# Kernel optimization log

Hardware: AMD Instinct MI355X
Metric: run time of the kernel (lower is better)

The kernel has to match this reference:

```python
import jax, jax.numpy as jnp
import numpy as np
from functools import partial
from jax import lax

B, K, CLIP_DIM, SBERT_DIM, D_MODEL, R_RANK, ATTN_DIM, PMAX = 128, 1024, 768, 384, 256, 64, 256, 8
RHO = 0.35

def _normalize(x, axis=-1, eps=1e-12):
    return x / jnp.maximum(jnp.linalg.norm(x, axis=axis, keepdims=True), eps)

def _build_graph():
    rng = np.random.default_rng(0)
    pid = np.zeros((K, PMAX), np.int32)
    pm = np.zeros((K, PMAX), bool)
    for i in range(K - 1):  # node i's parents are in (i, K); root = K-1 has none
        n = int(rng.integers(1, PMAX + 1))
        n = min(n, K - 1 - i)
        cands = rng.choice(np.arange(i + 1, K), size=n, replace=False)
        pid[i, :n] = cands
        pm[i, :n] = True
    order = np.arange(K - 1, -1, -1, dtype=np.int32)  # parents before children
    return jnp.asarray(pid), jnp.asarray(pm), jnp.asarray(order)

def setup_inputs() -> dict:
    key = jax.random.key(0)
    ks = iter(jax.random.split(key, 32))
    r = lambda shape, s=0.02: jax.random.normal(next(ks), shape, jnp.float32) * s
    pid, pm, order = _build_graph()
    return {
        "t_clip": jax.random.normal(next(ks), (B, CLIP_DIM), jnp.float32),
        "v_clip": jax.random.normal(next(ks), (B, CLIP_DIM), jnp.float32),
        "concept_sbert": jax.random.normal(next(ks), (K, SBERT_DIM), jnp.float32),
        "Wt": r((CLIP_DIM, D_MODEL)), "bt": jnp.zeros((D_MODEL,)),
        "Wv": r((CLIP_DIM, D_MODEL)), "bv": jnp.zeros((D_MODEL,)),
        "Wc": r((SBERT_DIM, D_MODEL)), "bc": jnp.zeros((D_MODEL,)),
        "Wp1": r((3 * D_MODEL, 2 * D_MODEL)), "bp1": jnp.zeros((2 * D_MODEL,)),
        "Wp2": r((2 * D_MODEL, D_MODEL)), "bp2": jnp.zeros((D_MODEL,)),
        "Wm1": r((3 * D_MODEL, 2 * D_MODEL)), "bm1": jnp.zeros((2 * D_MODEL,)),
        "Wm2": r((2 * D_MODEL, D_MODEL)), "bm2": jnp.zeros((D_MODEL,)),
        "tau_logits": jnp.zeros((K,)),
        "U": r((D_MODEL, R_RANK)), "V": r((D_MODEL, R_RANK)),
        "Wg1": r((SBERT_DIM, R_RANK)), "bg1": jnp.zeros((R_RANK,)),
        "Wg2": r((R_RANK, R_RANK)), "bg2": jnp.zeros((R_RANK,)),
        "w_out": r((K, R_RANK)), "b_out": jnp.zeros((K,)),
        "concept_q": r((K, ATTN_DIM)),
        "parents_idx": pid, "parents_mask": pm, "order": order,
    }

def _forward(t_clip, v_clip, concept_sbert, Wt, bt, Wv, bv, Wc, bc,
             Wp1, bp1, Wp2, bp2, Wm1, bm1, Wm2, bm2, tau_logits,
             U, V, Wg1, bg1, Wg2, bg2, w_out, b_out, concept_q,
             parents_idx, parents_mask, order):
    gelu = partial(jax.nn.gelu, approximate=False)  # torch nn.GELU default = exact erf
    t = _normalize(t_clip) @ Wt + bt                 # [B, D]
    v = _normalize(v_clip) @ Wv + bv                 # [B, D]
    d = concept_sbert @ Wc + bc                      # [K, D]
    # x = [v, t, d] broadcast to [B, K, 3D]
    x = jnp.concatenate([
        jnp.broadcast_to(v[:, None, :], (t.shape[0], K, D_MODEL)),
        jnp.broadcast_to(t[:, None, :], (t.shape[0], K, D_MODEL)),
        jnp.broadcast_to(d[None, :, :], (t.shape[0], K, D_MODEL)),
    ], axis=-1)
    h_plus = gelu(x @ Wp1 + bp1) @ Wp2 + bp2
    h_minus = gelu(x @ Wm1 + bm1) @ Wm2 + bm2
    tau = jax.nn.sigmoid(tau_logits)[None, :, None]
    h = tau * h_plus + (1.0 - tau) * h_minus         # [B, K, D]
    u = jnp.einsum('bkd,dr->bkr', h, U)
    vv = jnp.einsum('bkd,dr->bkr', h, V)
    g = gelu(concept_sbert @ Wg1 + bg1) @ Wg2 + bg2  # [K, R]
    inter = u * vv * g[None, :, :]
    logits = jnp.einsum('bkr,kr->bk', inter, w_out) + b_out[None, :]
    p = jax.nn.sigmoid(logits)                        # [B, K]
    # --- top-down hierarchical attention + multiplicative aggregation ---
    q = _normalize(concept_q)                         # [K, A]
    def step(p_hat, node):
        par = parents_idx[node]                       # [P] int
        m = parents_mask[node]                        # [P] bool
        scores = jnp.where(m, q[par] @ q[node], -1e9)
        alpha = jax.nn.softmax(scores)                # [P]
        vals = p_hat[:, par]                          # [B, P] gather of parent probs
        prod = jnp.prod(jnp.where(m[None, :], alpha[None, :] * vals, 1.0), axis=-1)
        new = jnp.where(m.any(), RHO * p[:, node] + (1.0 - RHO) * prod, p_hat[:, node])
        return p_hat.at[:, node].set(new), None       # scatter write
    p_hat, _ = lax.scan(step, p, order)
    return p_hat

def reference(t_clip, v_clip, concept_sbert, Wt, bt, Wv, bv, Wc, bc,
              Wp1, bp1, Wp2, bp2, Wm1, bm1, Wm2, bm2, tau_logits,
              U, V, Wg1, bg1, Wg2, bg2, w_out, b_out, concept_q,
              parents_idx, parents_mask, order):
    return _forward(t_clip, v_clip, concept_sbert, Wt, bt, Wv, bv, Wc, bc,
                    Wp1, bp1, Wp2, bp2, Wm1, bm1, Wm2, bm2, tau_logits,
                    U, V, Wg1, bg1, Wg2, bg2, w_out, b_out, concept_q,
                    parents_idx, parents_mask, order)
```

## Files before the change

### kernel.cpp

```cpp
#include <hip/hip_runtime.h>
#include <math.h>

typedef __attribute__((ext_vector_type(8))) short short8;
typedef __attribute__((ext_vector_type(4))) float float4v;
typedef __attribute__((ext_vector_type(2))) float float2v;

struct P {
  const float *t_clip, *v_clip, *sbert;
  const float *Wt, *bt, *Wv, *bv, *Wc, *bc;
  const float *Wp1, *bp1, *Wp2, *bp2, *Wm1, *bm1, *Wm2, *bm2;
  const float *tau_logits, *U, *V, *Wg1, *bg1, *Wg2, *bg2, *w_out, *b_out, *concept_q;
  const int *pid;
  float *vt32;
  unsigned short *vtbf;
  unsigned short *dbf;
  unsigned short *w1upP, *w1upM;
  unsigned short *w1lowP, *w1lowM;
  unsigned short *Ctp, *Ctm;
  unsigned short *Wpk, *Wmk;
  float *Ap, *Am;
  float *biasPM, *tau, *gw, *aprod;
  unsigned short *parS;
  int *sorted, *lvlStart, *nlev;
  float *pOut;
};

__device__ __forceinline__ unsigned short bf16ru(float f) {
    unsigned u = __float_as_uint(f);
    u += 0x7fffu + ((u >> 16) & 1u);
    return (unsigned short)(u >> 16);
}

__device__ __forceinline__ void glds16(const void* g, void* l) {
    __builtin_amdgcn_global_load_lds((const __attribute__((address_space(1))) unsigned int*)g,
                                     (__attribute__((address_space(3))) unsigned int*)l, 16, 0, 0);
}

__device__ __forceinline__ unsigned packpair(float2v a, unsigned c) {
    float2v cb;
    cb.x = __uint_as_float(c << 16);
    cb.y = __uint_as_float(c & 0xffff0000u);
    float2v x = a + cb;
    float2v t = x * x;
    float2v i = t * (-0.06649038f) + 0.39894228f;
    float2v p = x * i + 0.5f;
    float2v g = x * p;
    union { float2v f; unsigned u[2]; } gu; gu.f = g;
    return __builtin_amdgcn_perm(gu.u[1], gu.u[0], 0x07060302u);
}


__device__ void tv_f(const P& a, int rel, float* sm) {
    int sel = rel & 1, bt8 = rel >> 1;
    float* xrow = sm;
    float* scale = sm + 6144;
    int tid = threadIdx.x;
    const float* X = sel ? a.t_clip : a.v_clip;
    int b0 = bt8 * 8;
    for (int r = 0; r < 8; ++r)
        for (int i = tid; i < 768; i += 256)
            xrow[r * 768 + i] = X[(size_t)(b0 + r) * 768 + i];
    __syncthreads();
    {
        int r = tid >> 5, l = tid & 31;
        float ss = 0.f;
        for (int i = l; i < 768; i += 32) { float v = xrow[r * 768 + i]; ss = fmaf(v, v, ss); }
        for (int mk = 16; mk; mk >>= 1) ss += __shfl_xor(ss, mk);
        if (l == 0) scale[r] = 1.0f / fmaxf(sqrtf(ss), 1e-12f);
    }
    __syncthreads();
    int col4 = (tid & 63) * 4, rg = tid >> 6;
    const float* W = sel ? a.Wt : a.Wv;
    const float* bias = sel ? a.bt : a.bv;
    float acc[2][4] = {};
    const float* xr0 = xrow + (rg * 2) * 768;
    const float* xr1 = xr0 + 768;
    for (int d = 0; d < 768; ++d) {
        float4 w = *(const float4*)&W[(size_t)d * 256 + col4];
        float x0 = xr0[d], x1 = xr1[d];
        acc[0][0] = fmaf(x0, w.x, acc[0][0]); acc[0][1] = fmaf(x0, w.y, acc[0][1]);
        acc[0][2] = fmaf(x0, w.z, acc[0][2]); acc[0][3] = fmaf(x0, w.w, acc[0][3]);
        acc[1][0] = fmaf(x1, w.x, acc[1][0]); acc[1][1] = fmaf(x1, w.y, acc[1][1]);
        acc[1][2] = fmaf(x1, w.z, acc[1][2]); acc[1][3] = fmaf(x1, w.w, acc[1][3]);
    }
    float4 bb = *(const float4*)&bias[col4];
    int vtcol = sel * 256 + col4;
#pragma unroll
    for (int rr = 0; rr < 2; ++rr) {
        int b = b0 + rg * 2 + rr;
        float sc = scale[rg * 2 + rr];
        float4 o;
        o.x = acc[rr][0] * sc + bb.x; o.y = acc[rr][1] * sc + bb.y;
        o.z = acc[rr][2] * sc + bb.z; o.w = acc[rr][3] * sc + bb.w;
        *(float4*)&a.vt32[(size_t)b * 512 + vtcol] = o;
        ushort4 ob;
        ob.x = bf16ru(o.x); ob.y = bf16ru(o.y); ob.z = bf16ru(o.z); ob.w = bf16ru(o.w);
        size_t idx = (size_t)(b >> 4) * 8192 + (vtcol >> 5) * 512 + ((vtcol >> 3) & 3) * 128
                   + (b & 15) * 8 + (vtcol & 7);
        *(ushort4*)&a.vtbf[idx] = ob;
    }
}

__device__ void d_f(const P& a, int rel, float* sm) {
    int r0 = rel * 8;
    int tid = threadIdx.x;
    for (int i = tid; i < 3072; i += 256) sm[i] = a.sbert[(size_t)r0 * 384 + i];
    __syncthreads();
    int col4 = (tid & 63) * 4, rg = tid >> 6;
    float acc[2][4] = {};
    const float* x0p = sm + (rg * 2) * 384;
    const float* x1p = x0p + 384;
    for (int d = 0; d < 384; ++d) {
        float4 w = *(const float4*)&a.Wc[(size_t)d * 256 + col4];
        float x0 = x0p[d], x1 = x1p[d];
        acc[0][0] = fmaf(x0, w.x, acc[0][0]); acc[0][1] = fmaf(x0, w.y, acc[0][1]);
        acc[0][2] = fmaf(x0, w.z, acc[0][2]); acc[0][3] = fmaf(x0, w.w, acc[0][3]);
        acc[1][0] = fmaf(x1, w.x, acc[1][0]); acc[1][1] = fmaf(x1, w.y, acc[1][1]);
        acc[1][2] = fmaf(x1, w.z, acc[1][2]); acc[1][3] = fmaf(x1, w.w, acc[1][3]);
    }
    float4 bb = *(const float4*)&a.bc[col4];
#pragma unroll
    for (int rr = 0; rr < 2; ++rr) {
        int row = r0 + rg * 2 + rr;
        ushort4 ob;
        ob.x = bf16ru(acc[rr][0] + bb.x); ob.y = bf16ru(acc[rr][1] + bb.y);
        ob.z = bf16ru(acc[rr][2] + bb.z); ob.w = bf16ru(acc[rr][3] + bb.w);
        size_t idx = (size_t)(row >> 4) * 4096 + (col4 >> 5) * 512 + ((col4 >> 3) & 3) * 128
                   + (row & 15) * 8 + (col4 & 7);
        *(ushort4*)&a.dbf[idx] = ob;
    }
}

__device__ void wcv_f(const P& a, int rel, float* smf) {
    unsigned short* wl = (unsigned short*)smf;
    int mat = rel & 1, rb = rel >> 1;
    int r0 = rb * 16;
    const float* W1 = mat ? a.Wm1 : a.Wp1;
    int tid = threadIdx.x;
    for (int it = 0; it < 8; ++it) {
        int i4 = (it * 256 + tid) * 4;
        float4 w = *(const float4*)&W1[(size_t)r0 * 512 + i4];
        ushort4 o;
        o.x = bf16ru(w.x); o.y = bf16ru(w.y); o.z = bf16ru(w.z); o.w = bf16ru(w.w);
        *(ushort4*)&wl[i4] = o;
    }
    __syncthreads();
    unsigned short* dst; int K16, kbase;
    if (r0 < 512) { dst = mat ? a.w1upM : a.w1upP;  K16 = 8192; kbase = r0; }
    else          { dst = mat ? a.w1lowM : a.w1lowP; K16 = 4096; kbase = r0 - 512; }
    for (int i = tid; i < 1024; i += 256) {
        int kg = i >> 9, n = i & 511;
        int k0 = kbase + kg * 8;
        ushort4 o0, o1;
        o0.x = wl[(kg * 8 + 0) * 512 + n]; o0.y = wl[(kg * 8 + 1) * 512 + n];
        o0.z = wl[(kg * 8 + 2) * 512 + n]; o0.w = wl[(kg * 8 + 3) * 512 + n];
        o1.x = wl[(kg * 8 + 4) * 512 + n]; o1.y = wl[(kg * 8 + 5) * 512 + n];
        o1.z = wl[(kg * 8 + 6) * 512 + n]; o1.w = wl[(kg * 8 + 7) * 512 + n];
        size_t off = (size_t)(n >> 4) * K16 + (k0 >> 5) * 512 + ((k0 >> 3) & 3) * 128 + (n & 15) * 8;
        *(ushort4*)&dst[off]     = o0;
        *(ushort4*)&dst[off + 4] = o1;
    }
}

__device__ void packW_f(const P& a, int rel, float* smf) {
    float* w2l = smf;
    int mat = rel >> 6, jb = rel & 63;
    int j0 = jb * 8;
    const float* W2 = mat ? a.Wm2 : a.Wp2;
    unsigned short* outP = mat ? a.Wmk : a.Wpk;
    int tid = threadIdx.x;
    for (int i = tid; i < 2048; i += 256) w2l[i] = W2[(size_t)j0 * 256 + i];
    __syncthreads();
    int c = tid & 127, jg = tid >> 7;
    float acc[4] = {};
    const float* uv = (c < 64) ? (a.U + c) : (a.V + (c - 64));
    for (int d = 0; d < 256; ++d) {
        float u = uv[(size_t)d * 64];
        const float* wr = w2l + (jg * 4) * 256 + d;
        acc[0] = fmaf(wr[0],   u, acc[0]);
        acc[1] = fmaf(wr[256], u, acc[1]);
        acc[2] = fmaf(wr[512], u, acc[2]);
        acc[3] = fmaf(wr[768], u, acc[3]);
    }
#pragma unroll
    for (int r = 0; r < 4; ++r) {
        int j = j0 + jg * 4 + r;
        size_t o = (size_t)(j >> 5) * 4096 + (c >> 4) * 512 + ((j >> 3) & 3) * 128 + (c & 15) * 8 + (j & 7);
        outP[o] = bf16ru(acc[r]);
    }
}

__device__ void gw_f(const P& a, int rel, float* sm) {
    float* sb = sm;
    float* hid = sm + 6144;
    int k0 = rel * 16;
    int tid = threadIdx.x;
    for (int i = tid; i < 6144; i += 256) sb[i] = a.sbert[(size_t)k0 * 384 + i];
    __syncthreads();
    int col = tid & 63, rg = tid >> 6;
    float bg = a.bg1[col];
    float acc[4] = {bg, bg, bg, bg};
    for (int d = 0; d < 384; ++d) {
        float w = a.Wg1[(size_t)d * 64 + col];
        const float* xr = sb + (rg * 4) * 384 + d;
        acc[0] = fmaf(xr[0],    w, acc[0]);
        acc[1] = fmaf(xr[384],  w, acc[1]);
        acc[2] = fmaf(xr[768],  w, acc[2]);
        acc[3] = fmaf(xr[1152], w, acc[3]);
    }
#pragma unroll
    for (int r = 0; r < 4; ++r)
        hid[(rg * 4 + r) * 64 + col] = 0.5f * acc[r] * (1.0f + erff(acc[r] * 0.7071067811865475f));
    __syncthreads();
    float bg2v = a.bg2[col];
    float a2[4] = {bg2v, bg2v, bg2v, bg2v};
    for (int d = 0; d < 64; ++d) {
        float w = a.Wg2[(size_t)d * 64 + col];
        const float* hr = hid + (rg * 4) * 64 + d;
        a2[0] = fmaf(hr[0],   w, a2[0]);
        a2[1] = fmaf(hr[64],  w, a2[1]);
        a2[2] = fmaf(hr[128], w, a2[2]);
        a2[3] = fmaf(hr[192], w, a2[3]);
    }
#pragma unroll
    for (int r = 0; r < 4; ++r) {
        int k = k0 + rg * 4 + r;
        a.gw[(size_t)k * 64 + col] = a2[r] * a.w_out[(size_t)k * 64 + col];
    }
}

__device__ void alpha_f(const P& a, int blk) {
    int t = threadIdx.x, wv = t >> 6, lane = t & 63;
    int node = blk * 4 + wv;
    int slot = lane >> 3, e = lane & 7;
    int par = a.pid[node * 8 + slot];
    const float4* qk = (const float4*)(a.concept_q + (size_t)node * 256);
    const float4* qp = (const float4*)(a.concept_q + (size_t)par * 256);
    float dq = 0, np = 0, ns = 0;
#pragma unroll
    for (int i = 0; i < 8; ++i) {
        float4 x = qp[e * 8 + i], y = qk[e * 8 + i];
        dq += x.x * y.x + x.y * y.y + x.z * y.z + x.w * y.w;
        np += x.x * x.x + x.y * x.y + x.z * x.z + x.w * x.w;
        ns += y.x * y.x + y.y * y.y + y.z * y.z + y.w * y.w;
    }
#pragma unroll
    for (int mk = 1; mk <= 4; mk <<= 1) {
        dq += __shfl_xor(dq, mk); np += __shfl_xor(np, mk); ns += __shfl_xor(ns, mk);
    }
    float score = dq / fmaxf(sqrtf(np) * sqrtf(ns), 1e-24f);
    float sc[8]; int pv[8];
#pragma unroll
    for (int s = 0; s < 8; ++s) { sc[s] = __shfl(score, s * 8); pv[s] = __shfl(par, s * 8); }
    float mx = -1e30f;
#pragma unroll
    for (int s = 0; s < 8; ++s) if (pv[s] != 0) mx = fmaxf(mx, sc[s]);
    float sum = 0.f;
#pragma unroll
    for (int s = 0; s < 8; ++s) sum += (pv[s] != 0) ? expf(sc[s] - mx) : 0.0f;
    float ap = 1.0f;
#pragma unroll
    for (int s = 0; s < 8; ++s) if (pv[s] != 0) ap *= expf(sc[s] - mx) / sum;
    if (lane == 0) a.aprod[node] = ap;
    if (e == 0) a.parS[node * 8 + slot] = (par != 0) ? (unsigned short)par : (unsigned short)1024;
}

__device__ void misc_f(const P& a, int g) {
    int t = threadIdx.x;
    if (g == 0) {
        int c = t & 127;
        const float* bb = (t < 128) ? a.bp2 : a.bm2;
        const float* uv = (c < 64) ? (a.U + c) : (a.V + (c - 64));
        float acc = 0.f;
        for (int d = 0; d < 256; ++d) acc = fmaf(bb[d], uv[(size_t)d * 64], acc);
        a.biasPM[t] = acc;
    } else {
        int k = (g - 1) * 256 + t;
        a.tau[k] = 1.0f / (1.0f + expf(-a.tau_logits[k]));
    }
}

__device__ void levels_f(const P& a, int* smemI) {
    volatile int* lvl = smemI;
    int* cnt  = smemI + 1024;
    int* ofs  = smemI + 2048;
    int* ping = smemI + 3072;
    int* pong = smemI + 3328;
    int* mflag = smemI + 3584;
    int t = threadIdx.x;
    int par[4][8]; int hasm[4];
#pragma unroll
    for (int r = 0; r < 4; ++r) {
        int n = t * 4 + r, h = 0;
#pragma unroll
        for (int s = 0; s < 8; ++s) { int p = a.pid[n * 8 + s]; par[r][s] = p; h |= (p != 0); }
        hasm[r] = h; lvl[n] = 0;
    }
    if (t == 0) mflag[1] = 0;
    __syncthreads();
    for (int round = 0; round < 200; ++round) {
        if (t == 0) mflag[0] = 0;
        __syncthreads();
        int ch = 0;
        for (int sub = 0; sub < 8; ++sub) {
#pragma unroll
            for (int r = 0; r < 4; ++r) {
                if (!hasm[r]) continue;
                int mx = 0;
#pragma unroll
                for (int s = 0; s < 8; ++s) { int p = par[r][s]; if (p) mx = max(mx, lvl[p]); }
                int nl = mx + 1;
                if (nl > lvl[t * 4 + r]) { lvl[t * 4 + r] = nl; ch = 1; }
            }
        }
        if (ch) mflag[0] = 1;
        __syncthreads();
        if (mflag[0] == 0) break;
    }
    int lm = 0;
    for (int r = 0; r < 4; ++r) lm = max(lm, lvl[t * 4 + r]);
    atomicMax(&mflag[1], lm);
    for (int r = 0; r < 4; ++r) cnt[t * 4 + r] = 0;
    __syncthreads();
    for (int r = 0; r < 4; ++r) atomicAdd(&cnt[lvl[t * 4 + r]], 1);
    __syncthreads();
    int c0 = cnt[t * 4], c1 = cnt[t * 4 + 1], c2 = cnt[t * 4 + 2], c3 = cnt[t * 4 + 3];
    ping[t] = c0 + c1 + c2 + c3;
    __syncthreads();
    int* src = ping; int* dst = pong;
    for (int off = 1; off < 256; off <<= 1) {
        int v = src[t];
        if (t >= off) v += src[t - off];
        dst[t] = v;
        __syncthreads();
        int* tmp = src; src = dst; dst = tmp;
    }
    int excl = (t == 0) ? 0 : src[t - 1];
    ofs[t * 4] = excl; ofs[t * 4 + 1] = excl + c0;
    ofs[t * 4 + 2] = excl + c0 + c1; ofs[t * 4 + 3] = excl + c0 + c1 + c2;
#pragma unroll
    for (int r = 0; r < 4; ++r) a.lvlStart[t * 4 + r] = ofs[t * 4 + r];
    if (t == 0) { a.lvlStart[1024] = 1024; a.nlev[0] = mflag[1] + 1; }
    __syncthreads();
    for (int r = 0; r < 4; ++r) {
        int n = t * 4 + r;
        int pos = atomicAdd(&ofs[lvl[n]], 1);
        a.sorted[pos] = n;
    }
}

__global__ void __launch_bounds__(256) prep1_kernel(P a) {
    __shared__ float smem[7200];
    int bid = blockIdx.x;
    if (bid == 0) { levels_f(a, (int*)smem); return; }
    bid -= 1;
    if (bid < 32) { tv_f(a, bid, smem); return; }
    bid -= 32;
    if (bid < 128) { d_f(a, bid, smem); return; }
    bid -= 128;
    if (bid < 96) { wcv_f(a, bid, smem); return; }
    bid -= 96;
    if (bid < 128) { packW_f(a, bid, smem); return; }
    bid -= 128;
    if (bid < 64) { gw_f(a, bid, smem); return; }
    bid -= 64;
    if (bid < 256) { alpha_f(a, bid); return; }
    bid -= 256;
    misc_f(a, bid);
}

__global__ void __launch_bounds__(256) prep2_kernel(P a) {
    int bid = blockIdx.x;
    int tid = threadIdx.x;
    int wv = tid >> 6, lane = tid & 63;
    int m = lane & 15, quad = lane >> 4;
    if (bid < 256) {
        int mat = bid & 1, mt = (bid >> 1) & 15, ntile = bid >> 5;
        const unsigned short* A = a.dbf + (size_t)(mt * 4 + wv) * 4096 + quad * 128 + m * 8;
        const unsigned short* B = (mat ? a.w1lowM : a.w1lowP) + (size_t)quad * 128 + m * 8;
        unsigned short* Ct = mat ? a.Ctm : a.Ctp;
        float4v acc[4];
#pragma unroll
        for (int i = 0; i < 4; ++i) acc[i] = (float4v)0.0f;
        for (int s = 0; s < 8; ++s) {
            short8 af = *(const short8*)(A + s * 512);
#pragma unroll
            for (int nt = 0; nt < 4; ++nt) {
                short8 bf = *(const short8*)(B + (size_t)(ntile * 4 + nt) * 4096 + s * 512);
                acc[nt] = __builtin_amdgcn_mfma_f32_16x16x32_bf16(af, bf, acc[nt], 0, 0, 0);
            }
        }
        int rowg = mt * 4 + wv;
        int rl = quad * 4;
#pragma unroll
        for (int nt = 0; nt < 4; ++nt) {
            int j = ntile * 64 + nt * 16 + m;
            size_t base = (size_t)rowg * 8192 + (j >> 5) * 512 + ((j >> 3) & 3) * 128 + (j & 7);
#pragma unroll
            for (int rr = 0; rr < 4; ++rr)
                Ct[base + (rl + rr) * 8] = bf16ru(acc[nt][rr]);
        }
    } else {
        int rel = bid - 256;
        int mat = rel & 1, mt = (rel >> 1) & 1, ntile = rel >> 2;
        const unsigned short* A = a.vtbf + (size_t)(mt * 4 + wv) * 8192 + quad * 128 + m * 8;
        const unsigned short* B = (mat ? a.w1upM : a.w1upP) + (size_t)quad * 128 + m * 8;
        const float* bias = mat ? a.bm1 : a.bp1;
        float* out = mat ? a.Am : a.Ap;
        float4v acc[4];
#pragma unroll
        for (int i = 0; i < 4; ++i) acc[i] = (float4v)0.0f;
        for (int s = 0; s < 16; ++s) {
            short8 af = *(const short8*)(A + s * 512);
#pragma unroll
            for (int nt = 0; nt < 4; ++nt) {
                short8 bf = *(const short8*)(B + (size_t)(ntile * 4 + nt) * 8192 + s * 512);
                acc[nt] = __builtin_amdgcn_mfma_f32_16x16x32_bf16(af, bf, acc[nt], 0, 0, 0);
            }
        }
        int b0r = mt * 64 + wv * 16 + quad * 4;
#pragma unroll
        for (int nt = 0; nt < 4; ++nt) {
            int j = ntile * 64 + nt * 16 + m;
            float bb = bias[j];
#pragma unroll
            for (int rr = 0; rr < 4; ++rr)
                out[(size_t)(b0r + rr) * 512 + j] = acc[nt][rr] + bb;
        }
    }
}

__global__ void __launch_bounds__(512, 2) main_kernel(P a) {
    __shared__ float apL[4096];
    __shared__ char wbuf[2][16384];
    int tid = threadIdx.x;
    int wv2 = tid >> 6, lane = tid & 63;
    int mat = wv2 >> 2, sub = wv2 & 3;
    int m = lane & 15, quad = lane >> 4;
    int b0 = (blockIdx.x >> 4) * 4;
    int k0 = (blockIdx.x & 15) << 6;

    for (int i = tid; i < 1024; i += 512) {
        int arr = i >> 7, off = i & 127;
        const float* src = ((arr >> 2) ? a.Am : a.Ap) + (size_t)(b0 + (arr & 3)) * 512;
        ((float4*)apL)[i] = ((const float4*)src)[off];
    }

    const char* wg = ((wv2 < 4) ? (const char*)a.Wpk : (const char*)a.Wmk)
                   + (wv2 & 3) * 2048 + lane * 16;
    char* wl0 = &wbuf[0][wv2 * 2048];
    char* wl1 = &wbuf[1][wv2 * 2048];

    const unsigned short* Ct = mat ? a.Ctm : a.Ctp;
    const float* aL = apL + mat * 2048;
    int kt = (k0 >> 4) + sub;
    const char* ctB = (const char*)Ct + (size_t)kt * 16384 + quad * 256 + m * 16;

    float4v acc[4][8];
#pragma unroll
    for (int b = 0; b < 4; ++b)
#pragma unroll
        for (int i = 0; i < 8; ++i) acc[b][i] = (float4v)0.0f;

    glds16(wg, wl0);
    glds16(wg + 1024, wl0 + 1024);
    uint4 crN = *(const uint4*)(ctB);
    __syncthreads();

    for (int n = 0; n < 16; ++n) {
        if (n < 15) {
            char* dst = ((n + 1) & 1) ? wl1 : wl0;
            glds16(wg + (n + 1) * 8192, dst);
            glds16(wg + (n + 1) * 8192 + 1024, dst + 1024);
        }
        uint4 cr = crN;
        if (n < 15) crN = *(const uint4*)(ctB + (n + 1) * 1024);
        union { uint4 u; short8 s; } fa[4];
        const float* aj = aL + n * 32 + quad * 8;
#pragma unroll
        for (int b = 0; b < 4; ++b) {
            float4v x0 = *(const float4v*)(aj + b * 512);
            float4v x1 = *(const float4v*)(aj + b * 512 + 4);
            float2v v;
            v.x = x0[0]; v.y = x0[1]; fa[b].u.x = packpair(v, cr.x);
            v.x = x0[2]; v.y = x0[3]; fa[b].u.y = packpair(v, cr.y);
            v.x = x1[0]; v.y = x1[1]; fa[b].u.z = packpair(v, cr.z);
            v.x = x1[2]; v.y = x1[3]; fa[b].u.w = packpair(v, cr.w);
        }
        const char* wB = &wbuf[n & 1][0] + mat * 8192 + quad * 256 + m * 16;
#pragma unroll
        for (int nt = 0; nt < 8; ++nt) {
            short8 wf = *(const short8*)(wB + nt * 1024);
            acc[0][nt] = __builtin_amdgcn_mfma_f32_16x16x32_bf16(fa[0].s, wf, acc[0][nt], 0, 0, 0);
            acc[1][nt] = __builtin_amdgcn_mfma_f32_16x16x32_bf16(fa[1].s, wf, acc[1][nt], 0, 0, 0);
            acc[2][nt] = __builtin_amdgcn_mfma_f32_16x16x32_bf16(fa[2].s, wf, acc[2][nt], 0, 0, 0);
            acc[3][nt] = __builtin_amdgcn_mfma_f32_16x16x32_bf16(fa[3].s, wf, acc[3][nt], 0, 0, 0);
        }
        __syncthreads();
    }

    float* xbuf = (float*)wbuf;
    int kk[4]; float tv[4];
#pragma unroll
    for (int r = 0; r < 4; ++r) { kk[r] = k0 + sub * 16 + quad * 4 + r; tv[r] = a.tau[kk[r]]; }
    float lsum[4][4] = {};
#pragma unroll
    for (int t4 = 0; t4 < 4; ++t4) {
        __syncthreads();
        if (mat == 1) {
#pragma unroll
            for (int b = 0; b < 4; ++b) {
                int slot = (sub * 4 + b) * 64 + lane;
#pragma unroll
                for (int r = 0; r < 4; ++r) {
                    xbuf[r * 1024 + slot]       = acc[b][t4][r];
                    xbuf[(r + 4) * 1024 + slot] = acc[b][t4 + 4][r];
                }
            }
        }
        __syncthreads();
        if (mat == 0) {
            int cU = t4 * 16 + m, cV = cU + 64;
            float bPu = a.biasPM[cU], bMu = a.biasPM[128 + cU];
            float bPv = a.biasPM[cV], bMv = a.biasPM[128 + cV];
#pragma unroll
            for (int b = 0; b < 4; ++b) {
                int slot = (sub * 4 + b) * 64 + lane;
#pragma unroll
                for (int r = 0; r < 4; ++r) {
                    float g = a.gw[(size_t)kk[r] * 64 + cU];
                    float u  = tv[r] * (acc[b][t4][r] + bPu)
                             + (1.0f - tv[r]) * (xbuf[r * 1024 + slot] + bMu);
                    float vx = tv[r] * (acc[b][t4 + 4][r] + bPv)
                             + (1.0f - tv[r]) * (xbuf[(r + 4) * 1024 + slot] + bMv);
                    lsum[b][r] = fmaf(u * vx, g, lsum[b][r]);
                }
            }
        }
    }
    if (mat == 0) {
#pragma unroll
        for (int r = 0; r < 4; ++r) {
            float bo = a.b_out[kk[r]];
#pragma unroll
            for (int b = 0; b < 4; ++b) {
                float s = lsum[b][r];
                s += __shfl_xor(s, 1); s += __shfl_xor(s, 2); s += __shfl_xor(s, 4); s += __shfl_xor(s, 8);
                if (m == 0)
                    a.pOut[(size_t)(b0 + b) * 1024 + kk[r]] = 1.0f / (1.0f + expf(-(s + bo)));
            }
        }
    }
}

#define PH_STRIDE 1056
__global__ void __launch_bounds__(256) scan_kernel(P a) {
    __shared__ float ph[4 * PH_STRIDE];
    __shared__ float aprodL[1024];
    __shared__ unsigned short parL[8192];
    __shared__ short sortedL[1024];
    __shared__ int lvlStartL[1025];
    int t = threadIdx.x;
    int b0 = blockIdx.x * 4;
    for (int i = t; i < 1024; i += 256) ((uint4*)parL)[i] = ((const uint4*)a.parS)[i];
    for (int i = t; i < 1024; i += 256) {
        aprodL[i] = a.aprod[i];
        sortedL[i] = (short)a.sorted[i];
        lvlStartL[i] = a.lvlStart[i];
    }
    if (t == 0) lvlStartL[1024] = 1024;
    for (int i = t; i < 4096; i += 256) {
        int bb = i >> 10, k = i & 1023;
        ph[bb * PH_STRIDE + k] = a.pOut[(size_t)(b0 + bb) * 1024 + k];
    }
    if (t < 4) ph[t * PH_STRIDE + 1024] = 1.0f;
    __syncthreads();
    int nlev = a.nlev[0];
    int w = t >> 6, lane = t & 63;
    float* myph = ph + w * PH_STRIDE;
    for (int L = 1; L < nlev; ++L) {
        int s0 = lvlStartL[L], s1 = lvlStartL[L + 1];
        for (int i = s0 + lane; i < s1; i += 64) {
            int node = sortedL[i];
            ushort4 pA = *(const ushort4*)&parL[node * 8];
            ushort4 pB = *(const ushort4*)&parL[node * 8 + 4];
            float prod = aprodL[node];
            prod *= myph[pA.x] * myph[pA.y];
            prod *= myph[pA.z] * myph[pA.w];
            prod *= myph[pB.x] * myph[pB.y];
            prod *= myph[pB.z] * myph[pB.w];
            myph[node] = fmaf(0.35f, myph[node], 0.65f * prod);
        }
    }
    __syncthreads();
    for (int i = t; i < 4096; i += 256) {
        int bb = i >> 10, k = i & 1023;
        a.pOut[(size_t)(b0 + bb) * 1024 + k] = ph[bb * PH_STRIDE + k];
    }
}

extern "C" void kernel_launch(void* const* d_in, const int* in_sizes, int n_in,
                              void* d_out, int out_size, void* d_ws, size_t ws_size,
                              hipStream_t stream) {
    P a;
    a.t_clip = (const float*)d_in[0];
    a.v_clip = (const float*)d_in[1];
    a.sbert  = (const float*)d_in[2];
    a.Wt  = (const float*)d_in[3];  a.bt  = (const float*)d_in[4];
    a.Wv  = (const float*)d_in[5];  a.bv  = (const float*)d_in[6];
    a.Wc  = (const float*)d_in[7];  a.bc  = (const float*)d_in[8];
    a.Wp1 = (const float*)d_in[9];  a.bp1 = (const float*)d_in[10];
    a.Wp2 = (const float*)d_in[11]; a.bp2 = (const float*)d_in[12];
    a.Wm1 = (const float*)d_in[13]; a.bm1 = (const float*)d_in[14];
    a.Wm2 = (const float*)d_in[15]; a.bm2 = (const float*)d_in[16];
    a.tau_logits = (const float*)d_in[17];
    a.U   = (const float*)d_in[18]; a.V   = (const float*)d_in[19];
    a.Wg1 = (const float*)d_in[20]; a.bg1 = (const float*)d_in[21];
    a.Wg2 = (const float*)d_in[22]; a.bg2 = (const float*)d_in[23];
    a.w_out = (const float*)d_in[24]; a.b_out = (const float*)d_in[25];
    a.concept_q = (const float*)d_in[26];
    a.pid = (const int*)d_in[27];

    char* w = (char*)d_ws;
    a.vt32   = (float*)(w + 0);
    a.vtbf   = (unsigned short*)(w + 262144);
    a.dbf    = (unsigned short*)(w + 393216);
    a.w1upP  = (unsigned short*)(w + 917504);
    a.w1upM  = (unsigned short*)(w + 1441792);
    a.w1lowP = (unsigned short*)(w + 1966080);
    a.w1lowM = (unsigned short*)(w + 2228224);
    a.Ctp    = (unsigned short*)(w + 2490368);
    a.Ctm    = (unsigned short*)(w + 3538944);
    a.Wpk    = (unsigned short*)(w + 4587520);
    a.Wmk    = (unsigned short*)(w + 4718592);
    a.Ap     = (float*)(w + 4849664);
    a.Am     = (float*)(w + 5111808);
    a.biasPM = (float*)(w + 5373952);
    a.tau    = (float*)(w + 5374976);
    a.gw     = (float*)(w + 5379072);
    a.parS   = (unsigned short*)(w + 5641216);
    a.aprod  = (float*)(w + 5657600);
    a.sorted = (int*)(w + 5661696);
    a.lvlStart = (int*)(w + 5665792);
    a.nlev     = (int*)(w + 5670144);
    a.pOut = (float*)d_out;

    prep1_kernel<<<710, 256, 0, stream>>>(a);
    prep2_kernel<<<288, 256, 0, stream>>>(a);
    main_kernel<<<512, 512, 0, stream>>>(a);
    scan_kernel<<<32, 256, 0, stream>>>(a);
}
```

Baseline: 261.8 us.

## Move prep projections from scalar FP32 loops to bf16 MFMA GEMMs

```diff
diff --git a/kernel.cpp b/kernel.cpp
--- a/kernel.cpp
+++ b/kernel.cpp
@@ -11,15 +11,23 @@
   const float *Wp1, *bp1, *Wp2, *bp2, *Wm1, *bm1, *Wm2, *bm2;
   const float *tau_logits, *U, *V, *Wg1, *bg1, *Wg2, *bg2, *w_out, *b_out, *concept_q;
   const int *pid;
-  float *vt32;
+  unsigned short *tvbf;
+  unsigned short *sbbf;
+  unsigned short *wtvB;
+  unsigned short *wcB;
+  unsigned short *wg1B;
+  unsigned short *wg2B;
+  unsigned short *w2bf;
+  unsigned short *uvB;
+  unsigned short *w1upP, *w1upM;
+  unsigned short *w1lowP, *w1lowM;
   unsigned short *vtbf;
   unsigned short *dbf;
-  unsigned short *w1upP, *w1upM;
-  unsigned short *w1lowP, *w1lowM;
+  unsigned short *ghbf;
   unsigned short *Ctp, *Ctm;
   unsigned short *Wpk, *Wmk;
   float *Ap, *Am;
-  float *biasPM, *tau, *gw, *aprod;
+  float *sBuf, *biasPM, *tau, *gw, *aprod;
   unsigned short *parS;
   int *sorted, *lvlStart, *nlev;
   float *pOut;
@@ -50,183 +58,116 @@
 }
 
 
-__device__ void tv_f(const P& a, int rel, float* sm) {
-    int sel = rel & 1, bt8 = rel >> 1;
-    float* xrow = sm;
-    float* scale = sm + 6144;
+__device__ void bconv_f(const float* __restrict__ srcRow0, unsigned short* __restrict__ dst,
+                        int N, int K16, int kbase, char* smc) {
+    unsigned short* wl = (unsigned short*)smc;
     int tid = threadIdx.x;
-    const float* X = sel ? a.t_clip : a.v_clip;
-    int b0 = bt8 * 8;
-    for (int r = 0; r < 8; ++r)
-        for (int i = tid; i < 768; i += 256)
-            xrow[r * 768 + i] = X[(size_t)(b0 + r) * 768 + i];
-    __syncthreads();
-    {
-        int r = tid >> 5, l = tid & 31;
-        float ss = 0.f;
-        for (int i = l; i < 768; i += 32) { float v = xrow[r * 768 + i]; ss = fmaf(v, v, ss); }
-        for (int mk = 16; mk; mk >>= 1) ss += __shfl_xor(ss, mk);
-        if (l == 0) scale[r] = 1.0f / fmaxf(sqrtf(ss), 1e-12f);
-    }
-    __syncthreads();
-    int col4 = (tid & 63) * 4, rg = tid >> 6;
-    const float* W = sel ? a.Wt : a.Wv;
-    const float* bias = sel ? a.bt : a.bv;
-    float acc[2][4] = {};
-    const float* xr0 = xrow + (rg * 2) * 768;
-    const float* xr1 = xr0 + 768;
-    for (int d = 0; d < 768; ++d) {
-        float4 w = *(const float4*)&W[(size_t)d * 256 + col4];
-        float x0 = xr0[d], x1 = xr1[d];
-        acc[0][0] = fmaf(x0, w.x, acc[0][0]); acc[0][1] = fmaf(x0, w.y, acc[0][1]);
-        acc[0][2] = fmaf(x0, w.z, acc[0][2]); acc[0][3] = fmaf(x0, w.w, acc[0][3]);
-        acc[1][0] = fmaf(x1, w.x, acc[1][0]); acc[1][1] = fmaf(x1, w.y, acc[1][1]);
-        acc[1][2] = fmaf(x1, w.z, acc[1][2]); acc[1][3] = fmaf(x1, w.w, acc[1][3]);
-    }
-    float4 bb = *(const float4*)&bias[col4];
-    int vtcol = sel * 256 + col4;
-#pragma unroll
-    for (int rr = 0; rr < 2; ++rr) {
-        int b = b0 + rg * 2 + rr;
-        float sc = scale[rg * 2 + rr];
-        float4 o;
-        o.x = acc[rr][0] * sc + bb.x; o.y = acc[rr][1] * sc + bb.y;
-        o.z = acc[rr][2] * sc + bb.z; o.w = acc[rr][3] * sc + bb.w;
-        *(float4*)&a.vt32[(size_t)b * 512 + vtcol] = o;
-        ushort4 ob;
-        ob.x = bf16ru(o.x); ob.y = bf16ru(o.y); ob.z = bf16ru(o.z); ob.w = bf16ru(o.w);
-        size_t idx = (size_t)(b >> 4) * 8192 + (vtcol >> 5) * 512 + ((vtcol >> 3) & 3) * 128
-                   + (b & 15) * 8 + (vtcol & 7);
-        *(ushort4*)&a.vtbf[idx] = ob;
-    }
-}
-
-__device__ void d_f(const P& a, int rel, float* sm) {
-    int r0 = rel * 8;
-    int tid = threadIdx.x;
-    for (int i = tid; i < 3072; i += 256) sm[i] = a.sbert[(size_t)r0 * 384 + i];
-    __syncthreads();
-    int col4 = (tid & 63) * 4, rg = tid >> 6;
-    float acc[2][4] = {};
-    const float* x0p = sm + (rg * 2) * 384;
-    const float* x1p = x0p + 384;
-    for (int d = 0; d < 384; ++d) {
-        float4 w = *(const float4*)&a.Wc[(size_t)d * 256 + col4];
-        float x0 = x0p[d], x1 = x1p[d];
-        acc[0][0] = fmaf(x0, w.x, acc[0][0]); acc[0][1] = fmaf(x0, w.y, acc[0][1]);
-        acc[0][2] = fmaf(x0, w.z, acc[0][2]); acc[0][3] = fmaf(x0, w.w, acc[0][3]);
-        acc[1][0] = fmaf(x1, w.x, acc[1][0]); acc[1][1] = fmaf(x1, w.y, acc[1][1]);
-        acc[1][2] = fmaf(x1, w.z, acc[1][2]); acc[1][3] = fmaf(x1, w.w, acc[1][3]);
-    }
-    float4 bb = *(const float4*)&a.bc[col4];
-#pragma unroll
-    for (int rr = 0; rr < 2; ++rr) {
-        int row = r0 + rg * 2 + rr;
-        ushort4 ob;
-        ob.x = bf16ru(acc[rr][0] + bb.x); ob.y = bf16ru(acc[rr][1] + bb.y);
-        ob.z = bf16ru(acc[rr][2] + bb.z); ob.w = bf16ru(acc[rr][3] + bb.w);
-        size_t idx = (size_t)(row >> 4) * 4096 + (col4 >> 5) * 512 + ((col4 >> 3) & 3) * 128
-                   + (row & 15) * 8 + (col4 & 7);
-        *(ushort4*)&a.dbf[idx] = ob;
-    }
-}
-
-__device__ void wcv_f(const P& a, int rel, float* smf) {
-    unsigned short* wl = (unsigned short*)smf;
-    int mat = rel & 1, rb = rel >> 1;
-    int r0 = rb * 16;
-    const float* W1 = mat ? a.Wm1 : a.Wp1;
-    int tid = threadIdx.x;
-    for (int it = 0; it < 8; ++it) {
-        int i4 = (it * 256 + tid) * 4;
-        float4 w = *(const float4*)&W1[(size_t)r0 * 512 + i4];
+    int tot4 = 4 * N;
+    for (int i4 = tid; i4 < tot4; i4 += 256) {
+        float4 w = ((const float4*)srcRow0)[i4];
         ushort4 o;
         o.x = bf16ru(w.x); o.y = bf16ru(w.y); o.z = bf16ru(w.z); o.w = bf16ru(w.w);
-        *(ushort4*)&wl[i4] = o;
-    }
-    __syncthreads();
-    unsigned short* dst; int K16, kbase;
-    if (r0 < 512) { dst = mat ? a.w1upM : a.w1upP;  K16 = 8192; kbase = r0; }
-    else          { dst = mat ? a.w1lowM : a.w1lowP; K16 = 4096; kbase = r0 - 512; }
-    for (int i = tid; i < 1024; i += 256) {
-        int kg = i >> 9, n = i & 511;
+        *(ushort4*)&wl[i4 * 4] = o;
+    }
+    __syncthreads();
+    for (int i = tid; i < 2 * N; i += 256) {
+        int kg = (i >= N) ? 1 : 0;
+        int n = i - kg * N;
         int k0 = kbase + kg * 8;
         ushort4 o0, o1;
-        o0.x = wl[(kg * 8 + 0) * 512 + n]; o0.y = wl[(kg * 8 + 1) * 512 + n];
-        o0.z = wl[(kg * 8 + 2) * 512 + n]; o0.w = wl[(kg * 8 + 3) * 512 + n];
-        o1.x = wl[(kg * 8 + 4) * 512 + n]; o1.y = wl[(kg * 8 + 5) * 512 + n];
-        o1.z = wl[(kg * 8 + 6) * 512 + n]; o1.w = wl[(kg * 8 + 7) * 512 + n];
+        o0.x = wl[(kg * 8 + 0) * N + n]; o0.y = wl[(kg * 8 + 1) * N + n];
+        o0.z = wl[(kg * 8 + 2) * N + n]; o0.w = wl[(kg * 8 + 3) * N + n];
+        o1.x = wl[(kg * 8 + 4) * N + n]; o1.y = wl[(kg * 8 + 5) * N + n];
+        o1.z = wl[(kg * 8 + 6) * N + n]; o1.w = wl[(kg * 8 + 7) * N + n];
         size_t off = (size_t)(n >> 4) * K16 + (k0 >> 5) * 512 + ((k0 >> 3) & 3) * 128 + (n & 15) * 8;
         *(ushort4*)&dst[off]     = o0;
         *(ushort4*)&dst[off + 4] = o1;
     }
 }
 
-__device__ void packW_f(const P& a, int rel, float* smf) {
-    float* w2l = smf;
-    int mat = rel >> 6, jb = rel & 63;
-    int j0 = jb * 8;
-    const float* W2 = mat ? a.Wm2 : a.Wp2;
-    unsigned short* outP = mat ? a.Wmk : a.Wpk;
+__device__ void aconv_f(const float* __restrict__ src, unsigned short* __restrict__ dst,
+                        int r0, int K, int K16) {
     int tid = threadIdx.x;
-    for (int i = tid; i < 2048; i += 256) w2l[i] = W2[(size_t)j0 * 256 + i];
-    __syncthreads();
-    int c = tid & 127, jg = tid >> 7;
-    float acc[4] = {};
+    int Kq = K >> 2;
+    for (int rl = 0; rl < 16; ++rl) {
+        int row = r0 + rl;
+        for (int i = tid; i < Kq; i += 256) {
+            float4 w = ((const float4*)(src + (size_t)row * K))[i];
+            ushort4 o;
+            o.x = bf16ru(w.x); o.y = bf16ru(w.y); o.z = bf16ru(w.z); o.w = bf16ru(w.w);
+            int k4 = i * 4;
+            size_t off = (size_t)(row >> 4) * K16 + (k4 >> 5) * 512 + ((k4 >> 3) & 3) * 128
+                       + (row & 15) * 8 + (k4 & 7);
+            *(ushort4*)&dst[off] = o;
+        }
+    }
+}
+
+__device__ void tcv_f(const P& a, int rel) {
+    int sel = rel & 1, r8 = rel >> 1;
+    const float* X = sel ? a.t_clip : a.v_clip;
+    unsigned short* dst = a.tvbf + sel * 98304;
+    int tid = threadIdx.x;
+    int rl = tid >> 5, l = tid & 31;
+    int b = r8 * 8 + rl;
+    const float4* src = (const float4*)(X + (size_t)b * 768);
+    float ss = 0.f;
+#pragma unroll
+    for (int j = 0; j < 6; ++j) {
+        int i4 = l + j * 32;
+        float4 w = src[i4];
+        ss += w.x * w.x + w.y * w.y + w.z * w.z + w.w * w.w;
+        ushort4 o;
+        o.x = bf16ru(w.x); o.y = bf16ru(w.y); o.z = bf16ru(w.z); o.w = bf16ru(w.w);
+        int k4 = i4 * 4;
+        size_t off = (size_t)(b >> 4) * 12288 + (k4 >> 5) * 512 + ((k4 >> 3) & 3) * 128
+                   + (b & 15) * 8 + (k4 & 7);
+        *(ushort4*)&dst[off] = o;
+    }
+#pragma unroll
+    for (int mk = 16; mk; mk >>= 1) ss += __shfl_xor(ss, mk);
+    if (l == 0) a.sBuf[sel * 128 + b] = 1.0f / fmaxf(sqrtf(ss), 1e-12f);
+}
+
+__device__ void uvconv_f(const P& a, int blk, char* smc) {
+    unsigned short* wl = (unsigned short*)smc;
+    int kbase = blk * 16;
+    int tid = threadIdx.x;
+    for (int i = tid; i < 2048; i += 256) {
+        int kl = i >> 7, n = i & 127;
+        float v = (n < 64) ? a.U[(size_t)(kbase + kl) * 64 + n]
+                           : a.V[(size_t)(kbase + kl) * 64 + (n - 64)];
+        wl[kl * 128 + n] = bf16ru(v);
+    }
+    __syncthreads();
+    {
+        int i = tid;
+        int kg = i >> 7, n = i & 127;
+        int k0 = kbase + kg * 8;
+        ushort4 o0, o1;
+        o0.x = wl[(kg * 8 + 0) * 128 + n]; o0.y = wl[(kg * 8 + 1) * 128 + n];
+        o0.z = wl[(kg * 8 + 2) * 128 + n]; o0.w = wl[(kg * 8 + 3) * 128 + n];
+        o1.x = wl[(kg * 8 + 4) * 128 + n]; o1.y = wl[(kg * 8 + 5) * 128 + n];
+        o1.z = wl[(kg * 8 + 6) * 128 + n]; o1.w = wl[(kg * 8 + 7) * 128 + n];
+        size_t off = (size_t)(n >> 4) * 4096 + (k0 >> 5) * 512 + ((k0 >> 3) & 3) * 128 + (n & 15) * 8;
+        *(ushort4*)&a.uvB[off]     = o0;
+        *(ushort4*)&a.uvB[off + 4] = o1;
+    }
+}
+
+__device__ void biasPM_f(const P& a, int blk) {
+    int tid = threadIdx.x;
+    int o = blk * 32 + (tid >> 3), e = tid & 7;
+    const float* bb = (o < 128) ? a.bp2 : a.bm2;
+    int c = o & 127;
     const float* uv = (c < 64) ? (a.U + c) : (a.V + (c - 64));
-    for (int d = 0; d < 256; ++d) {
-        float u = uv[(size_t)d * 64];
-        const float* wr = w2l + (jg * 4) * 256 + d;
-        acc[0] = fmaf(wr[0],   u, acc[0]);
-        acc[1] = fmaf(wr[256], u, acc[1]);
-        acc[2] = fmaf(wr[512], u, acc[2]);
-        acc[3] = fmaf(wr[768], u, acc[3]);
-    }
-#pragma unroll
-    for (int r = 0; r < 4; ++r) {
-        int j = j0 + jg * 4 + r;
-        size_t o = (size_t)(j >> 5) * 4096 + (c >> 4) * 512 + ((j >> 3) & 3) * 128 + (c & 15) * 8 + (j & 7);
-        outP[o] = bf16ru(acc[r]);
-    }
-}
-
-__device__ void gw_f(const P& a, int rel, float* sm) {
-    float* sb = sm;
-    float* hid = sm + 6144;
-    int k0 = rel * 16;
-    int tid = threadIdx.x;
-    for (int i = tid; i < 6144; i += 256) sb[i] = a.sbert[(size_t)k0 * 384 + i];
-    __syncthreads();
-    int col = tid & 63, rg = tid >> 6;
-    float bg = a.bg1[col];
-    float acc[4] = {bg, bg, bg, bg};
-    for (int d = 0; d < 384; ++d) {
-        float w = a.Wg1[(size_t)d * 64 + col];
-        const float* xr = sb + (rg * 4) * 384 + d;
-        acc[0] = fmaf(xr[0],    w, acc[0]);
-        acc[1] = fmaf(xr[384],  w, acc[1]);
-        acc[2] = fmaf(xr[768],  w, acc[2]);
-        acc[3] = fmaf(xr[1152], w, acc[3]);
-    }
-#pragma unroll
-    for (int r = 0; r < 4; ++r)
-        hid[(rg * 4 + r) * 64 + col] = 0.5f * acc[r] * (1.0f + erff(acc[r] * 0.7071067811865475f));
-    __syncthreads();
-    float bg2v = a.bg2[col];
-    float a2[4] = {bg2v, bg2v, bg2v, bg2v};
-    for (int d = 0; d < 64; ++d) {
-        float w = a.Wg2[(size_t)d * 64 + col];
-        const float* hr = hid + (rg * 4) * 64 + d;
-        a2[0] = fmaf(hr[0],   w, a2[0]);
-        a2[1] = fmaf(hr[64],  w, a2[1]);
-        a2[2] = fmaf(hr[128], w, a2[2]);
-        a2[3] = fmaf(hr[192], w, a2[3]);
-    }
-#pragma unroll
-    for (int r = 0; r < 4; ++r) {
-        int k = k0 + rg * 4 + r;
-        a.gw[(size_t)k * 64 + col] = a2[r] * a.w_out[(size_t)k * 64 + col];
-    }
+    float acc = 0.f;
+    for (int d = e * 32; d < e * 32 + 32; ++d)
+        acc = fmaf(bb[d], uv[(size_t)d * 64], acc);
+    acc += __shfl_xor(acc, 1);
+    acc += __shfl_xor(acc, 2);
+    acc += __shfl_xor(acc, 4);
+    if (e == 0) a.biasPM[o] = acc;
 }
 
 __device__ void alpha_f(const P& a, int blk) {
@@ -263,21 +204,6 @@
     for (int s = 0; s < 8; ++s) if (pv[s] != 0) ap *= expf(sc[s] - mx) / sum;
     if (lane == 0) a.aprod[node] = ap;
     if (e == 0) a.parS[node * 8 + slot] = (par != 0) ? (unsigned short)par : (unsigned short)1024;
-}
-
-__device__ void misc_f(const P& a, int g) {
-    int t = threadIdx.x;
-    if (g == 0) {
-        int c = t & 127;
-        const float* bb = (t < 128) ? a.bp2 : a.bm2;
-        const float* uv = (c < 64) ? (a.U + c) : (a.V + (c - 64));
-        float acc = 0.f;
-        for (int d = 0; d < 256; ++d) acc = fmaf(bb[d], uv[(size_t)d * 64], acc);
-        a.biasPM[t] = acc;
-    } else {
-        int k = (g - 1) * 256 + t;
-        a.tau[k] = 1.0f / (1.0f + expf(-a.tau_logits[k]));
-    }
 }
 
 __device__ void levels_f(const P& a, int* smemI) {
@@ -349,24 +275,157 @@
     }
 }
 
-__global__ void __launch_bounds__(256) prep1_kernel(P a) {
-    __shared__ float smem[7200];
+__global__ void __launch_bounds__(256) prep0_kernel(P a) {
+    __shared__ char smem[16640];
     int bid = blockIdx.x;
     if (bid == 0) { levels_f(a, (int*)smem); return; }
     bid -= 1;
-    if (bid < 32) { tv_f(a, bid, smem); return; }
+    if (bid < 96) {
+        int mat = bid & 1, rb = bid >> 1;
+        int r0 = rb * 16;
+        const float* W1 = mat ? a.Wm1 : a.Wp1;
+        if (r0 < 512) bconv_f(W1 + (size_t)r0 * 512, mat ? a.w1upM : a.w1upP, 512, 8192, r0, smem);
+        else          bconv_f(W1 + (size_t)r0 * 512, mat ? a.w1lowM : a.w1lowP, 512, 4096, r0 - 512, smem);
+        return;
+    }
+    bid -= 96;
+    if (bid < 96) {
+        int sel = bid & 1, ch = bid >> 1;
+        bconv_f((sel ? a.Wt : a.Wv) + (size_t)ch * 16 * 256, a.wtvB + sel * 196608, 256, 12288, ch * 16, smem);
+        return;
+    }
+    bid -= 96;
+    if (bid < 24) { bconv_f(a.Wc + (size_t)bid * 16 * 256, a.wcB, 256, 6144, bid * 16, smem); return; }
+    bid -= 24;
+    if (bid < 24) { bconv_f(a.Wg1 + (size_t)bid * 16 * 64, a.wg1B, 64, 6144, bid * 16, smem); return; }
+    bid -= 24;
+    if (bid < 4) { bconv_f(a.Wg2 + (size_t)bid * 16 * 64, a.wg2B, 64, 1024, bid * 16, smem); return; }
+    bid -= 4;
+    if (bid < 64) {
+        int mat = bid & 1, ch = bid >> 1;
+        aconv_f(mat ? a.Wm2 : a.Wp2, a.w2bf + mat * 131072, ch * 16, 256, 4096);
+        return;
+    }
+    bid -= 64;
+    if (bid < 16) { uvconv_f(a, bid, smem); return; }
+    bid -= 16;
+    if (bid < 32) { tcv_f(a, bid); return; }
     bid -= 32;
-    if (bid < 128) { d_f(a, bid, smem); return; }
-    bid -= 128;
-    if (bid < 96) { wcv_f(a, bid, smem); return; }
-    bid -= 96;
-    if (bid < 128) { packW_f(a, bid, smem); return; }
-    bid -= 128;
-    if (bid < 64) { gw_f(a, bid, smem); return; }
+    if (bid < 64) { aconv_f(a.sbert, a.sbbf, bid * 16, 384, 6144); return; }
     bid -= 64;
     if (bid < 256) { alpha_f(a, bid); return; }
     bid -= 256;
-    misc_f(a, bid);
+    if (bid < 8) { biasPM_f(a, bid); return; }
+    bid -= 8;
+    { int k = bid * 256 + threadIdx.x; a.tau[k] = 1.0f / (1.0f + expf(-a.tau_logits[k])); }
+}
+
+__device__ __forceinline__ void gemm64(const unsigned short* A, const unsigned short* B,
+                                       int K16A, int K16B, int nsteps,
+                                       float4v acc[4], int m, int quad) {
+    const unsigned short* Ab = A + quad * 128 + m * 8;
+    const unsigned short* Bb = B + quad * 128 + m * 8;
+    for (int s = 0; s < nsteps; ++s) {
+        short8 af = *(const short8*)(Ab + s * 512);
+#pragma unroll
+        for (int nt = 0; nt < 4; ++nt) {
+            short8 bf = *(const short8*)(Bb + (size_t)nt * K16B + s * 512);
+            acc[nt] = __builtin_amdgcn_mfma_f32_16x16x32_bf16(af, bf, acc[nt], 0, 0, 0);
+        }
+    }
+}
+
+__global__ void __launch_bounds__(256) prep1_kernel(P a) {
+    int bid = blockIdx.x;
+    int tid = threadIdx.x;
+    int wv = tid >> 6, lane = tid & 63;
+    int m = lane & 15, quad = lane >> 4;
+    float4v acc[4];
+#pragma unroll
+    for (int i = 0; i < 4; ++i) acc[i] = (float4v)0.0f;
+
+    if (bid < 16) {
+        int sel = bid & 1, mt = (bid >> 1) & 1, ntile = bid >> 2;
+        const unsigned short* A = a.tvbf + sel * 98304 + (size_t)(mt * 4 + wv) * 12288;
+        const unsigned short* B = a.wtvB + sel * 196608 + (size_t)(ntile * 4) * 12288;
+        gemm64(A, B, 12288, 12288, 24, acc, m, quad);
+        const float* bias = sel ? a.bt : a.bv;
+#pragma unroll
+        for (int nt = 0; nt < 4; ++nt) {
+            int col = ntile * 64 + nt * 16 + m;
+            int vtcol = sel * 256 + col;
+            float bb = bias[col];
+#pragma unroll
+            for (int r = 0; r < 4; ++r) {
+                int row = mt * 64 + wv * 16 + quad * 4 + r;
+                float val = acc[nt][r] * a.sBuf[sel * 128 + row] + bb;
+                size_t off = (size_t)(row >> 4) * 8192 + (vtcol >> 5) * 512
+                           + ((vtcol >> 3) & 3) * 128 + (row & 15) * 8 + (vtcol & 7);
+                a.vtbf[off] = bf16ru(val);
+            }
+        }
+        return;
+    }
+    bid -= 16;
+    if (bid < 64) {
+        int mt = bid & 15, ntile = bid >> 4;
+        const unsigned short* A = a.sbbf + (size_t)(mt * 4 + wv) * 6144;
+        const unsigned short* B = a.wcB + (size_t)(ntile * 4) * 6144;
+        gemm64(A, B, 6144, 6144, 12, acc, m, quad);
+#pragma unroll
+        for (int nt = 0; nt < 4; ++nt) {
+            int col = ntile * 64 + nt * 16 + m;
+            float bb = a.bc[col];
+#pragma unroll
+            for (int r = 0; r < 4; ++r) {
+                int row = mt * 64 + wv * 16 + quad * 4 + r;
+                size_t off = (size_t)(row >> 4) * 4096 + (col >> 5) * 512
+                           + ((col >> 3) & 3) * 128 + (row & 15) * 8 + (col & 7);
+                a.dbf[off] = bf16ru(acc[nt][r] + bb);
+            }
+        }
+        return;
+    }
+    bid -= 64;
+    if (bid < 16) {
+        int mt = bid;
+        const unsigned short* A = a.sbbf + (size_t)(mt * 4 + wv) * 6144;
+        gemm64(A, a.wg1B, 6144, 6144, 12, acc, m, quad);
+#pragma unroll
+        for (int nt = 0; nt < 4; ++nt) {
+            int col = nt * 16 + m;
+            float bb = a.bg1[col];
+#pragma unroll
+            for (int r = 0; r < 4; ++r) {
+                int row = mt * 64 + wv * 16 + quad * 4 + r;
+                float x = acc[nt][r] + bb;
+                float g = 0.5f * x * (1.0f + erff(x * 0.7071067811865475f));
+                size_t off = (size_t)(row >> 4) * 1024 + (col >> 5) * 512
+                           + ((col >> 3) & 3) * 128 + (row & 15) * 8 + (col & 7);
+                a.ghbf[off] = bf16ru(g);
+            }
+        }
+        return;
+    }
+    bid -= 16;
+    {
+        int mat = bid & 1, mt = (bid >> 1) & 7, ntile = bid >> 4;
+        const unsigned short* A = a.w2bf + mat * 131072 + (size_t)(mt * 4 + wv) * 4096;
+        const unsigned short* B = a.uvB + (size_t)(ntile * 4) * 4096;
+        gemm64(A, B, 4096, 4096, 8, acc, m, quad);
+        unsigned short* outP = mat ? a.Wmk : a.Wpk;
+#pragma unroll
+        for (int nt = 0; nt < 4; ++nt) {
+            int c = ntile * 64 + nt * 16 + m;
+#pragma unroll
+            for (int r = 0; r < 4; ++r) {
+                int j = mt * 64 + wv * 16 + quad * 4 + r;
+                size_t o = (size_t)(j >> 5) * 4096 + (c >> 4) * 512 + ((j >> 3) & 3) * 128
+                         + (c & 15) * 8 + (j & 7);
+                outP[o] = bf16ru(acc[nt][r]);
+            }
+        }
+    }
 }
 
 __global__ void __launch_bounds__(256) prep2_kernel(P a) {
@@ -400,9 +459,11 @@
             for (int rr = 0; rr < 4; ++rr)
                 Ct[base + (rl + rr) * 8] = bf16ru(acc[nt][rr]);
         }
-    } else {
-        int rel = bid - 256;
-        int mat = rel & 1, mt = (rel >> 1) & 1, ntile = rel >> 2;
+        return;
+    }
+    bid -= 256;
+    if (bid < 32) {
+        int mat = bid & 1, mt = (bid >> 1) & 1, ntile = bid >> 2;
         const unsigned short* A = a.vtbf + (size_t)(mt * 4 + wv) * 8192 + quad * 128 + m * 8;
         const unsigned short* B = (mat ? a.w1upM : a.w1upP) + (size_t)quad * 128 + m * 8;
         const float* bias = mat ? a.bm1 : a.bp1;
@@ -426,6 +487,34 @@
 #pragma unroll
             for (int rr = 0; rr < 4; ++rr)
                 out[(size_t)(b0r + rr) * 512 + j] = acc[nt][rr] + bb;
+        }
+        return;
+    }
+    bid -= 32;
+    {
+        int mt = bid;
+        const unsigned short* A = a.ghbf + (size_t)(mt * 4 + wv) * 1024 + quad * 128 + m * 8;
+        const unsigned short* B = a.wg2B + (size_t)quad * 128 + m * 8;
+        float4v acc[4];
+#pragma unroll
+        for (int i = 0; i < 4; ++i) acc[i] = (float4v)0.0f;
+        for (int s = 0; s < 2; ++s) {
+            short8 af = *(const short8*)(A + s * 512);
+#pragma unroll
+            for (int nt = 0; nt < 4; ++nt) {
+                short8 bf = *(const short8*)(B + (size_t)nt * 1024 + s * 512);
+                acc[nt] = __builtin_amdgcn_mfma_f32_16x16x32_bf16(af, bf, acc[nt], 0, 0, 0);
+            }
+        }
+#pragma unroll
+        for (int nt = 0; nt < 4; ++nt) {
+            int col = nt * 16 + m;
+            float bb = a.bg2[col];
+#pragma unroll
+            for (int r = 0; r < 4; ++r) {
+                int k = mt * 64 + wv * 16 + quad * 4 + r;
+                a.gw[(size_t)k * 64 + col] = (acc[nt][r] + bb) * a.w_out[(size_t)k * 64 + col];
+            }
         }
     }
 }
@@ -622,31 +711,41 @@
     a.pid = (const int*)d_in[27];
 
     char* w = (char*)d_ws;
-    a.vt32   = (float*)(w + 0);
-    a.vtbf   = (unsigned short*)(w + 262144);
-    a.dbf    = (unsigned short*)(w + 393216);
-    a.w1upP  = (unsigned short*)(w + 917504);
-    a.w1upM  = (unsigned short*)(w + 1441792);
-    a.w1lowP = (unsigned short*)(w + 1966080);
-    a.w1lowM = (unsigned short*)(w + 2228224);
-    a.Ctp    = (unsigned short*)(w + 2490368);
-    a.Ctm    = (unsigned short*)(w + 3538944);
-    a.Wpk    = (unsigned short*)(w + 4587520);
-    a.Wmk    = (unsigned short*)(w + 4718592);
-    a.Ap     = (float*)(w + 4849664);
-    a.Am     = (float*)(w + 5111808);
-    a.biasPM = (float*)(w + 5373952);
-    a.tau    = (float*)(w + 5374976);
-    a.gw     = (float*)(w + 5379072);
-    a.parS   = (unsigned short*)(w + 5641216);
-    a.aprod  = (float*)(w + 5657600);
-    a.sorted = (int*)(w + 5661696);
-    a.lvlStart = (int*)(w + 5665792);
-    a.nlev     = (int*)(w + 5670144);
+    a.Ctp  = (unsigned short*)(w + 0);
+    a.Ctm  = (unsigned short*)(w + 1048576);
+    a.tvbf = (unsigned short*)(w + 0);
+    a.sbbf = (unsigned short*)(w + 393216);
+    a.wtvB = (unsigned short*)(w + 1179648);
+    a.wcB  = (unsigned short*)(w + 1966080);
+    a.w1upP  = (unsigned short*)(w + 2162688);
+    a.w1upM  = (unsigned short*)(w + 2686976);
+    a.w1lowP = (unsigned short*)(w + 3211264);
+    a.w1lowM = (unsigned short*)(w + 3473408);
+    a.wg1B   = (unsigned short*)(w + 3735552);
+    a.wg2B   = (unsigned short*)(w + 3784704);
+    a.w2bf   = (unsigned short*)(w + 3792896);
+    a.uvB    = (unsigned short*)(w + 4317184);
+    a.vtbf   = (unsigned short*)(w + 4382720);
+    a.dbf    = (unsigned short*)(w + 4513792);
+    a.ghbf   = (unsigned short*)(w + 5038080);
+    a.Wpk    = (unsigned short*)(w + 5169152);
+    a.Wmk    = (unsigned short*)(w + 5300224);
+    a.Ap     = (float*)(w + 5431296);
+    a.Am     = (float*)(w + 5693440);
+    a.biasPM = (float*)(w + 5955584);
+    a.tau    = (float*)(w + 5956608);
+    a.gw     = (float*)(w + 5960704);
+    a.sBuf   = (float*)(w + 6222848);
+    a.parS   = (unsigned short*)(w + 6223872);
+    a.aprod  = (float*)(w + 6240256);
+    a.sorted = (int*)(w + 6244352);
+    a.lvlStart = (int*)(w + 6248448);
+    a.nlev     = (int*)(w + 6252672);
     a.pOut = (float*)d_out;
 
-    prep1_kernel<<<710, 256, 0, stream>>>(a);
-    prep2_kernel<<<288, 256, 0, stream>>>(a);
+    prep0_kernel<<<689, 256, 0, stream>>>(a);
+    prep1_kernel<<<128, 256, 0, stream>>>(a);
+    prep2_kernel<<<304, 256, 0, stream>>>(a);
     main_kernel<<<512, 512, 0, stream>>>(a);
     scan_kernel<<<32, 256, 0, stream>>>(a);
 }
```

Result: slower. 276.6 us (+5.7%).
